# Kernel optimization log

Measured on AMD Instinct MI355X. Metric: run time of the kernel, lower is better.

Reference implementation:

```python
import jax, jax.numpy as jnp
import numpy as np

HIDDEN = 1024
STATE = 16
EXPAND = 2
INNER = HIDDEN * EXPAND
BATCH, SEQ = 4, 2048


def setup_inputs() -> dict:
    key = jax.random.key(0)
    ks = jax.random.split(key, 12)
    s = 0.02
    return {
        "x": jax.random.normal(ks[0], (BATCH, SEQ, HIDDEN), jnp.float32),
        "norm_scale": jnp.ones((HIDDEN,), jnp.float32),
        "norm_bias": jnp.zeros((HIDDEN,), jnp.float32),
        "W_in": jax.random.normal(ks[1], (HIDDEN, 2 * INNER), jnp.float32) * s,
        "conv_w": jax.random.normal(ks[2], (INNER, 3), jnp.float32) * 0.3,
        "conv_b": jnp.zeros((INNER,), jnp.float32),
        "W_dt": jax.random.normal(ks[3], (INNER, INNER), jnp.float32) * s,
        "b_dt": jnp.zeros((INNER,), jnp.float32),
        "A_log": jax.random.normal(ks[4], (INNER, STATE), jnp.float32),
        "D_param": jnp.ones((INNER,), jnp.float32),
        "W_B": jax.random.normal(ks[5], (INNER, STATE), jnp.float32) * s,
        "W_C": jax.random.normal(ks[6], (INNER, STATE), jnp.float32) * s,
        "W_out": jax.random.normal(ks[7], (INNER, HIDDEN), jnp.float32) * s,
    }


def reference(x, norm_scale, norm_bias, W_in, conv_w, conv_b, W_dt, b_dt,
              A_log, D_param, W_B, W_C, W_out):
    residual = x
    # LayerNorm (eps = 1e-5, matches nn.LayerNorm default)
    mu = jnp.mean(x, axis=-1, keepdims=True)
    var = jnp.mean(jnp.square(x - mu), axis=-1, keepdims=True)
    xn = (x - mu) * jax.lax.rsqrt(var + 1e-5) * norm_scale + norm_bias

    xz = xn @ W_in                         # [B, L, 2*inner]
    xb, z = jnp.split(xz, 2, axis=-1)      # each [B, L, inner]

    # depthwise conv1d, kernel 3, padding 1 (cross-correlation as in torch)
    xp = jnp.pad(xb, ((0, 0), (1, 1), (0, 0)))
    xb = (conv_w[:, 0] * xp[:, :-2] + conv_w[:, 1] * xp[:, 1:-1]
          + conv_w[:, 2] * xp[:, 2:] + conv_b)
    xb = jax.nn.silu(xb)

    dt = jax.nn.softplus(xb @ W_dt + b_dt)  # [B, L, inner]
    A = -jnp.exp(A_log)                     # [inner, N]
    Bi = xb @ W_B                           # [B, L, N]
    Ci = xb @ W_C                           # [B, L, N]

    def step(h, inp):
        x_t, dt_t, B_t, C_t = inp           # [B,D], [B,D], [B,N], [B,N]
        A_bar = jnp.exp(dt_t[:, :, None] * A)                 # [B, D, N]
        h = A_bar * h + (dt_t * x_t)[:, :, None] * B_t[:, None, :]
        y_t = jnp.einsum('bdn,bn->bd', h, C_t)
        return h, y_t

    h0 = jnp.zeros((x.shape[0], INNER, STATE), x.dtype)
    xs = (jnp.swapaxes(xb, 0, 1), jnp.swapaxes(dt, 0, 1),
          jnp.swapaxes(Bi, 0, 1), jnp.swapaxes(Ci, 0, 1))
    _, y = jax.lax.scan(step, h0, xs)       # y: [L, B, D]
    y = jnp.swapaxes(y, 0, 1)

    y = (y + D_param * xb) * jax.nn.silu(z)
    return residual + y @ W_out
```

## Files before the change

kernel.cpp:

```cpp
#include <hip/hip_runtime.h>
#include <hip/hip_bf16.h>
#include <cstdint>
#include <cstddef>

#define B_DIM 4
#define L_DIM 2048
#define H_DIM 1024
#define D_DIM 2048
#define N_STATE 16
#define TOKENS (B_DIM * L_DIM)
#define CH 32
#define LC (L_DIM / CH)
#define NEXT 2176

typedef __bf16 bf16x8 __attribute__((ext_vector_type(8)));
typedef float f32x4 __attribute__((ext_vector_type(4)));

__device__ __forceinline__ float sigmoidf_(float x) { return 1.f / (1.f + __expf(-x)); }
__device__ __forceinline__ float softplusf_(float x) {
  return fmaxf(x, 0.f) + log1pf(__expf(-fabsf(x)));
}
__device__ __forceinline__ void gl_lds16(const void* g, void* l) {
  __builtin_amdgcn_global_load_lds(
      (const __attribute__((address_space(1))) unsigned int*)g,
      (__attribute__((address_space(3))) unsigned int*)l, 16, 0, 0);
}

__global__ __launch_bounds__(256) void ln_kernel(const float* __restrict__ x,
    const float* __restrict__ gamma, const float* __restrict__ beta,
    __hip_bfloat16* __restrict__ out) {
  int row = blockIdx.x;
  int t = threadIdx.x;
  const float* px = x + (size_t)row * H_DIM;
  float4 v = *(const float4*)(px + t * 4);
  float s  = v.x + v.y + v.z + v.w;
  float ss = v.x * v.x + v.y * v.y + v.z * v.z + v.w * v.w;
  for (int off = 32; off > 0; off >>= 1) {
    s  += __shfl_down(s, off);
    ss += __shfl_down(ss, off);
  }
  __shared__ float red[8];
  __shared__ float stats[2];
  int wave = t >> 6, lane = t & 63;
  if (lane == 0) { red[wave] = s; red[4 + wave] = ss; }
  __syncthreads();
  if (t == 0) {
    float S  = red[0] + red[1] + red[2] + red[3];
    float SS = red[4] + red[5] + red[6] + red[7];
    float mu = S / H_DIM;
    float var = SS / H_DIM - mu * mu;
    stats[0] = mu;
    stats[1] = rsqrtf(var + 1e-5f);
  }
  __syncthreads();
  float mu = stats[0], rstd = stats[1];
  float4 g  = *(const float4*)(gamma + t * 4);
  float4 bt = *(const float4*)(beta + t * 4);
  __hip_bfloat16* po = out + (size_t)row * H_DIM + t * 4;
  po[0] = __float2bfloat16((v.x - mu) * rstd * g.x + bt.x);
  po[1] = __float2bfloat16((v.y - mu) * rstd * g.y + bt.y);
  po[2] = __float2bfloat16((v.z - mu) * rstd * g.z + bt.z);
  po[3] = __float2bfloat16((v.w - mu) * rstd * g.w + bt.w);
}

__global__ void transpose_bf16(const float* __restrict__ in,
                               __hip_bfloat16* __restrict__ out, int R, int C) {
  __shared__ float tile[32][33];
  int c0 = blockIdx.x * 32, r0 = blockIdx.y * 32;
  int tx = threadIdx.x, ty = threadIdx.y;
  for (int i = 0; i < 32; i += 8)
    tile[ty + i][tx] = in[(size_t)(r0 + ty + i) * C + c0 + tx];
  __syncthreads();
  for (int i = 0; i < 32; i += 8)
    out[(size_t)(c0 + ty + i) * R + r0 + tx] = __float2bfloat16(tile[tx][ty + i]);
}

__global__ __launch_bounds__(256) void wbc_transpose(const float* __restrict__ WB,
    const float* __restrict__ WC, __hip_bfloat16* __restrict__ Wext) {
  int tid = blockIdx.x * 256 + threadIdx.x;
  int c = tid & 31;
  int k0 = (tid >> 5) * 16;
  const float* W = (c < 16) ? WB : WC;
  int cc = c & 15;
  __hip_bfloat16* o = Wext + (size_t)(2048 + c) * D_DIM + k0;
  for (int kk = 0; kk < 16; ++kk)
    o[kk] = __float2bfloat16(W[(size_t)(k0 + kk) * N_STATE + cc]);
}

#define BM 128
#define BN 128
#define BK 64

template <int MODE>
__global__ __launch_bounds__(256) void gemm_bf16(
    const __hip_bfloat16* __restrict__ A, const __hip_bfloat16* __restrict__ Bt,
    void* __restrict__ C0, void* __restrict__ C1, int nsplit,
    int K, int lda, int ldb, int ldc, int gx,
    const float* __restrict__ bias, const float* __restrict__ resid) {
  __shared__ __hip_bfloat16 As[2 * BM * BK];
  __shared__ __hip_bfloat16 Bs[2 * BN * BK];
  int t = threadIdx.x;
  int bid = blockIdx.x;
  int nsup = gx << 3;
  int super = bid / nsup;
  int rem = bid - super * nsup;
  int m0 = (super * 8 + (rem & 7)) * BM;
  int n0 = (rem >> 3) * BN;

  int wave = t >> 6, lane = t & 63;
  int quad = lane >> 4, l16 = lane & 15;
  int wm = (wave >> 1) * 64, wn = (wave & 1) * 64;

  f32x4 acc[4][4] = {};

  int srow  = t >> 3;
  int cslot = t & 7;
  int cdata = cslot ^ (srow & 7);
  const __hip_bfloat16* Ag[4];
  const __hip_bfloat16* Bg[4];
  int soff[4];
#pragma unroll
  for (int j = 0; j < 4; ++j) {
    Ag[j]  = A  + (size_t)(m0 + j * 32 + srow) * lda + cdata * 8;
    Bg[j]  = Bt + (size_t)(n0 + j * 32 + srow) * ldb + cdata * 8;
    soff[j] = (j * 32 + srow) * BK + cslot * 8;
  }

  const int NT = K / BK;
#pragma unroll
  for (int j = 0; j < 4; ++j) {
    gl_lds16(Ag[j], &As[soff[j]]);
    gl_lds16(Bg[j], &Bs[soff[j]]);
  }
  asm volatile("s_waitcnt vmcnt(0)" ::: "memory");
  __builtin_amdgcn_s_barrier();

  for (int kt = 0; kt < NT; ++kt) {
    const int cur = (kt & 1) * (BM * BK);
    const int nxt = cur ^ (BM * BK);
    if (kt + 1 < NT) {
      const int k1 = (kt + 1) * BK;
#pragma unroll
      for (int j = 0; j < 4; ++j) {
        gl_lds16(Ag[j] + k1, &As[nxt + soff[j]]);
        gl_lds16(Bg[j] + k1, &Bs[nxt + soff[j]]);
      }
    }
#pragma unroll
    for (int s = 0; s < 2; ++s) {
      int cs = ((s * 4 + quad) ^ (l16 & 7)) * 8;
      bf16x8 af[4], bf_[4];
#pragma unroll
      for (int i = 0; i < 4; ++i) {
        af[i]  = *(const bf16x8*)&As[cur + (wm + i * 16 + l16) * BK + cs];
        bf_[i] = *(const bf16x8*)&Bs[cur + (wn + i * 16 + l16) * BK + cs];
      }
#pragma unroll
      for (int i = 0; i < 4; ++i)
#pragma unroll
        for (int j = 0; j < 4; ++j)
          acc[i][j] = __builtin_amdgcn_mfma_f32_16x16x32_bf16(af[i], bf_[j], acc[i][j], 0, 0, 0);
    }
    asm volatile("s_waitcnt vmcnt(0)" ::: "memory");
    __builtin_amdgcn_s_barrier();
  }

#pragma unroll
  for (int i = 0; i < 4; ++i) {
    int row0 = m0 + wm + i * 16 + quad * 4;
#pragma unroll
    for (int j = 0; j < 4; ++j) {
      int col = n0 + wn + j * 16 + l16;
      f32x4 v = acc[i][j];
      if (MODE == 0) {
#pragma unroll
        for (int r = 0; r < 4; ++r) {
          size_t idx = (size_t)(row0 + r) * ldc + col;
          ((float*)C0)[idx] = v[r] + resid[idx];
        }
      } else if (MODE == 1) {
        bool mainc = (col < nsplit);
        __hip_bfloat16* cb = mainc ? (__hip_bfloat16*)C0 : (__hip_bfloat16*)C1;
        int ccol = mainc ? col : col - nsplit;
#pragma unroll
        for (int r = 0; r < 4; ++r)
          cb[(size_t)(row0 + r) * ldc + ccol] = __float2bfloat16(v[r]);
      } else {
        if (col < nsplit) {
          float bb = bias[col];
#pragma unroll
          for (int r = 0; r < 4; ++r)
            ((__hip_bfloat16*)C0)[(size_t)(row0 + r) * ldc + col] =
                __float2bfloat16(softplusf_(v[r] + bb));
        } else {
#pragma unroll
          for (int r = 0; r < 4; ++r)
            ((float*)C1)[(size_t)(row0 + r) * 128 + (col - nsplit)] = v[r];
        }
      }
    }
  }
}

__global__ __launch_bounds__(256) void conv_silu_kernel(const __hip_bfloat16* __restrict__ xb,
    const float* __restrict__ cw, const float* __restrict__ cb,
    __hip_bfloat16* __restrict__ xbc) {
  size_t i2 = (size_t)blockIdx.x * 256 + threadIdx.x;
  int dp = (int)(i2 & (D_DIM / 2 - 1));
  size_t tok = i2 >> 10;
  int l = (int)(tok & (L_DIM - 1));
  int d = dp * 2;
  const __hip_bfloat162* base = (const __hip_bfloat162*)xb + i2;
  __hip_bfloat162 cc = base[0];
  float v0 = cw[d * 3 + 1] * __bfloat162float(cc.x) + cb[d];
  float v1 = cw[d * 3 + 4] * __bfloat162float(cc.y) + cb[d + 1];
  if (l > 0) {
    __hip_bfloat162 pm = base[-(D_DIM / 2)];
    v0 += cw[d * 3 + 0] * __bfloat162float(pm.x);
    v1 += cw[d * 3 + 3] * __bfloat162float(pm.y);
  }
  if (l < L_DIM - 1) {
    __hip_bfloat162 pp = base[D_DIM / 2];
    v0 += cw[d * 3 + 2] * __bfloat162float(pp.x);
    v1 += cw[d * 3 + 5] * __bfloat162float(pp.y);
  }
  v0 = v0 * sigmoidf_(v0);
  v1 = v1 * sigmoidf_(v1);
  __hip_bfloat162 o;
  o.x = __float2bfloat16(v0);
  o.y = __float2bfloat16(v1);
  ((__hip_bfloat162*)xbc)[i2] = o;
}

__global__ __launch_bounds__(256) void scan1_kernel(const __hip_bfloat16* __restrict__ dt,
    const __hip_bfloat16* __restrict__ xbc, const float* __restrict__ BiCi,
    const float* __restrict__ A_log, float* __restrict__ hfin,
    float* __restrict__ dtsum) {
  __shared__ float Bsh[LC * N_STATE];
  int t = threadIdx.x;
  int d = blockIdx.x * 256 + t;
  int c = blockIdx.y, b = blockIdx.z;
  size_t base = (size_t)b * L_DIM + (size_t)c * LC;
  for (int idx = t; idx < LC * 4; idx += 256) {
    int row = idx >> 2, q = idx & 3;
    ((float4*)Bsh)[row * 4 + q] = *(const float4*)&BiCi[(base + row) * 128 + q * 4];
  }
  float Aneg[N_STATE];
  {
    const float4* Ap = (const float4*)(A_log + (size_t)d * N_STATE);
#pragma unroll
    for (int q = 0; q < 4; ++q) {
      float4 av = Ap[q];
      Aneg[4 * q + 0] = -__expf(av.x);
      Aneg[4 * q + 1] = -__expf(av.y);
      Aneg[4 * q + 2] = -__expf(av.z);
      Aneg[4 * q + 3] = -__expf(av.w);
    }
  }
  __syncthreads();
  const __hip_bfloat16* dtp = dt + base * D_DIM + d;
  const __hip_bfloat16* xp = xbc + base * D_DIM + d;
  float h[N_STATE];
#pragma unroll
  for (int n = 0; n < N_STATE; ++n) h[n] = 0.f;
  float ds = 0.f;
  float dtv = __bfloat162float(dtp[0]), xv = __bfloat162float(xp[0]);
  for (int i = 0; i < LC; ++i) {
    int ip = (i < LC - 1) ? i + 1 : i;
    float dt2 = __bfloat162float(dtp[(size_t)ip * D_DIM]);
    float x2  = __bfloat162float(xp[(size_t)ip * D_DIM]);
    float dtx = dtv * xv;
    ds += dtv;
    const float4* Brow = (const float4*)&Bsh[i * N_STATE];
#pragma unroll
    for (int q = 0; q < 4; ++q) {
      float4 bv = Brow[q];
      h[4*q+0] = __expf(dtv * Aneg[4*q+0]) * h[4*q+0] + dtx * bv.x;
      h[4*q+1] = __expf(dtv * Aneg[4*q+1]) * h[4*q+1] + dtx * bv.y;
      h[4*q+2] = __expf(dtv * Aneg[4*q+2]) * h[4*q+2] + dtx * bv.z;
      h[4*q+3] = __expf(dtv * Aneg[4*q+3]) * h[4*q+3] + dtx * bv.w;
    }
    dtv = dt2; xv = x2;
  }
  float* ho = hfin + (((size_t)b * CH + c) * D_DIM + d) * N_STATE;
#pragma unroll
  for (int q = 0; q < 4; ++q) {
    float4 v; v.x = h[4*q]; v.y = h[4*q+1]; v.z = h[4*q+2]; v.w = h[4*q+3];
    ((float4*)ho)[q] = v;
  }
  dtsum[((size_t)b * CH + c) * D_DIM + d] = ds;
}

__global__ __launch_bounds__(256) void scan2_kernel(const float* __restrict__ hfin,
    const float* __restrict__ dtsum, const float* __restrict__ A_log,
    float* __restrict__ hstart) {
  int tid = blockIdx.x * 256 + threadIdx.x;
  int n = tid & 15;
  int d = (tid >> 4) & (D_DIM - 1);
  int b = tid >> 15;
  float Aneg = -__expf(A_log[d * N_STATE + n]);
  float run = 0.f;
  for (int c = 0; c < CH; ++c) {
    size_t o = (((size_t)b * CH + c) * D_DIM + d) * N_STATE + n;
    hstart[o] = run;
    run = __expf(Aneg * dtsum[((size_t)b * CH + c) * D_DIM + d]) * run + hfin[o];
  }
}

__global__ __launch_bounds__(256) void scan3_kernel(const __hip_bfloat16* __restrict__ dt,
    const __hip_bfloat16* __restrict__ xbc, const float* __restrict__ BiCi,
    const float* __restrict__ A_log,
    const float* __restrict__ hstart, const __hip_bfloat16* __restrict__ z,
    const float* __restrict__ Dp, __hip_bfloat16* __restrict__ yo) {
  __shared__ float Bsh[LC * N_STATE];
  __shared__ float Csh[LC * N_STATE];
  int t = threadIdx.x;
  int d = blockIdx.x * 256 + t;
  int c = blockIdx.y, b = blockIdx.z;
  size_t base = (size_t)b * L_DIM + (size_t)c * LC;
  for (int idx = t; idx < LC * 4; idx += 256) {
    int row = idx >> 2, q = idx & 3;
    ((float4*)Bsh)[row * 4 + q] = *(const float4*)&BiCi[(base + row) * 128 + q * 4];
    ((float4*)Csh)[row * 4 + q] = *(const float4*)&BiCi[(base + row) * 128 + 16 + q * 4];
  }
  float Aneg[N_STATE];
  {
    const float4* Ap = (const float4*)(A_log + (size_t)d * N_STATE);
#pragma unroll
    for (int q = 0; q < 4; ++q) {
      float4 av = Ap[q];
      Aneg[4 * q + 0] = -__expf(av.x);
      Aneg[4 * q + 1] = -__expf(av.y);
      Aneg[4 * q + 2] = -__expf(av.z);
      Aneg[4 * q + 3] = -__expf(av.w);
    }
  }
  float h[N_STATE];
  {
    const float4* hs = (const float4*)(hstart + (((size_t)b * CH + c) * D_DIM + d) * N_STATE);
#pragma unroll
    for (int q = 0; q < 4; ++q) {
      float4 v = hs[q];
      h[4*q] = v.x; h[4*q+1] = v.y; h[4*q+2] = v.z; h[4*q+3] = v.w;
    }
  }
  float Dv = Dp[d];
  __syncthreads();
  const __hip_bfloat16* dtp = dt + base * D_DIM + d;
  const __hip_bfloat16* xp = xbc + base * D_DIM + d;
  const __hip_bfloat16* zp = z + base * D_DIM + d;
  __hip_bfloat16* yp = yo + base * D_DIM + d;
  float dtv = __bfloat162float(dtp[0]), xv = __bfloat162float(xp[0]);
  float zv = __bfloat162float(zp[0]);
  for (int i = 0; i < LC; ++i) {
    int ip = (i < LC - 1) ? i + 1 : i;
    float dt2 = __bfloat162float(dtp[(size_t)ip * D_DIM]);
    float x2  = __bfloat162float(xp[(size_t)ip * D_DIM]);
    float z2  = __bfloat162float(zp[(size_t)ip * D_DIM]);
    float dtx = dtv * xv;
    const float4* Brow = (const float4*)&Bsh[i * N_STATE];
    const float4* Crow = (const float4*)&Csh[i * N_STATE];
    float yv = 0.f;
#pragma unroll
    for (int q = 0; q < 4; ++q) {
      float4 bv = Brow[q];
      float4 cv = Crow[q];
      h[4*q+0] = __expf(dtv * Aneg[4*q+0]) * h[4*q+0] + dtx * bv.x;
      h[4*q+1] = __expf(dtv * Aneg[4*q+1]) * h[4*q+1] + dtx * bv.y;
      h[4*q+2] = __expf(dtv * Aneg[4*q+2]) * h[4*q+2] + dtx * bv.z;
      h[4*q+3] = __expf(dtv * Aneg[4*q+3]) * h[4*q+3] + dtx * bv.w;
      yv += h[4*q+0] * cv.x + h[4*q+1] * cv.y + h[4*q+2] * cv.z + h[4*q+3] * cv.w;
    }
    float g = zv * sigmoidf_(zv);
    yp[(size_t)i * D_DIM] = __float2bfloat16((yv + Dv * xv) * g);
    dtv = dt2; xv = x2; zv = z2;
  }
}

extern "C" void kernel_launch(void* const* d_in, const int* in_sizes, int n_in,
                              void* d_out, int out_size, void* d_ws, size_t ws_size,
                              hipStream_t stream) {
  const float* x          = (const float*)d_in[0];
  const float* norm_scale = (const float*)d_in[1];
  const float* norm_bias  = (const float*)d_in[2];
  const float* W_in       = (const float*)d_in[3];
  const float* conv_w     = (const float*)d_in[4];
  const float* conv_b     = (const float*)d_in[5];
  const float* W_dt       = (const float*)d_in[6];
  const float* b_dt       = (const float*)d_in[7];
  const float* A_log      = (const float*)d_in[8];
  const float* D_param    = (const float*)d_in[9];
  const float* W_B        = (const float*)d_in[10];
  const float* W_C        = (const float*)d_in[11];
  const float* W_out      = (const float*)d_in[12];
  float* out = (float*)d_out;

  const size_t MB = 1024 * 1024;
  const size_t NEEDED = 193 * MB;
  if (ws_size < NEEDED) return;

  char* ws = (char*)d_ws;
  __hip_bfloat16* xn     = (__hip_bfloat16*)(ws);
  __hip_bfloat16* W_outT = (__hip_bfloat16*)(ws);
  __hip_bfloat16* xb     = (__hip_bfloat16*)(ws + 16 * MB);
  __hip_bfloat16* ybf    = (__hip_bfloat16*)(ws + 16 * MB);
  __hip_bfloat16* z      = (__hip_bfloat16*)(ws + 48 * MB);
  __hip_bfloat16* xbc    = (__hip_bfloat16*)(ws + 80 * MB);
  __hip_bfloat16* dtY    = (__hip_bfloat16*)(ws + 112 * MB);
  float*          BiCi   = (float*)(ws + 144 * MB);
  __hip_bfloat16* W_ext  = (__hip_bfloat16*)(ws + 148 * MB);
  float*          hstart = (float*)(ws + 158 * MB);
  float*          dtsum  = (float*)(ws + 174 * MB);
  __hip_bfloat16* W_inT  = (__hip_bfloat16*)(ws + 177 * MB);
  float*          hfin   = (float*)(ws + 177 * MB);

  dim3 tb(32, 8);
  transpose_bf16<<<dim3(4096 / 32, 1024 / 32), tb, 0, stream>>>(W_in, W_inT, 1024, 4096);
  transpose_bf16<<<dim3(2048 / 32, 2048 / 32), tb, 0, stream>>>(W_dt, W_ext, 2048, 2048);
  wbc_transpose<<<16, 256, 0, stream>>>(W_B, W_C, W_ext);
  ln_kernel<<<TOKENS, 256, 0, stream>>>(x, norm_scale, norm_bias, xn);
  gemm_bf16<1><<<(4096 / BN) * (TOKENS / BM), 256, 0, stream>>>(
      xn, W_inT, xb, z, D_DIM, H_DIM, H_DIM, H_DIM, D_DIM, 4096 / BN,
      nullptr, nullptr);
  transpose_bf16<<<dim3(1024 / 32, 2048 / 32), tb, 0, stream>>>(W_out, W_outT, 2048, 1024);
  conv_silu_kernel<<<(TOKENS * D_DIM / 2) / 256, 256, 0, stream>>>(xb, conv_w, conv_b, xbc);
  gemm_bf16<2><<<(NEXT / BN) * (TOKENS / BM), 256, 0, stream>>>(
      xbc, W_ext, dtY, BiCi, D_DIM, D_DIM, D_DIM, D_DIM, D_DIM, NEXT / BN,
      b_dt, nullptr);
  scan1_kernel<<<dim3(D_DIM / 256, CH, B_DIM), 256, 0, stream>>>(
      dtY, xbc, BiCi, A_log, hfin, dtsum);
  scan2_kernel<<<(B_DIM * D_DIM * N_STATE) / 256, 256, 0, stream>>>(
      hfin, dtsum, A_log, hstart);
  scan3_kernel<<<dim3(D_DIM / 256, CH, B_DIM), 256, 0, stream>>>(
      dtY, xbc, BiCi, A_log, hstart, z, D_param, ybf);
  gemm_bf16<0><<<(H_DIM / BN) * (TOKENS / BM), 256, 0, stream>>>(
      ybf, W_outT, out, nullptr, 1 << 30, D_DIM, D_DIM, D_DIM, H_DIM, H_DIM / BN,
      nullptr, x);
}
```

Measured before the change: 575.5 us.

## Add 256x256-tile bf16 MFMA GEMM and use it for input and dt/B/C projections

Introduces a 512-thread GEMM kernel with 256x256 output tiles, swizzled LDS staging via direct global-to-LDS loads, and double buffering, replacing the 128x128 GEMM for the input projection and the fused dt/B/C projection. Larger tiles raise arithmetic intensity and reduce global traffic per FLOP. The extended-weight width is padded to a multiple of 256, with output writes clipped by a column limit. Risks include lower occupancy from the large LDS footprint and tail imbalance from fewer, larger workgroups.

```diff
diff --git a/kernel.cpp b/kernel.cpp
--- a/kernel.cpp
+++ b/kernel.cpp
@@ -11,7 +11,8 @@
 #define TOKENS (B_DIM * L_DIM)
 #define CH 32
 #define LC (L_DIM / CH)
-#define NEXT 2176
+#define NEXT 2304
+#define NLIM2 2080
 
 typedef __bf16 bf16x8 __attribute__((ext_vector_type(8)));
 typedef float f32x4 __attribute__((ext_vector_type(4)));
@@ -85,6 +86,126 @@
   __hip_bfloat16* o = Wext + (size_t)(2048 + c) * D_DIM + k0;
   for (int kk = 0; kk < 16; ++kk)
     o[kk] = __float2bfloat16(W[(size_t)(k0 + kk) * N_STATE + cc]);
+}
+
+#define BK256 64
+
+template <int MODE>
+__global__ __launch_bounds__(512, 2) void gemm256(
+    const __hip_bfloat16* __restrict__ A, const __hip_bfloat16* __restrict__ Bt,
+    void* __restrict__ C0, void* __restrict__ C1, int nsplit, int nlimit,
+    int K, int lda, int ldb, int ldc, int ntn,
+    const float* __restrict__ bias, const float* __restrict__ resid) {
+  __shared__ __hip_bfloat16 lds[65536];
+  const int t = threadIdx.x;
+  const int nwg = gridDim.x;
+  int bid = blockIdx.x;
+  int wgid = (bid & 7) * (nwg >> 3) + (bid >> 3);
+  const int m0 = (wgid / ntn) * 256;
+  const int n0 = (wgid % ntn) * 256;
+
+  const int wave = t >> 6, lane = t & 63;
+  const int wm = wave >> 2, wn = wave & 3;
+  const int l16 = lane & 15, quad = lane >> 4;
+
+  const int srow = t >> 3, cslot = t & 7;
+  const int cdata = cslot ^ (srow & 7);
+  const __hip_bfloat16* Ag = A + (size_t)(m0 + srow) * lda + cdata * 8;
+  const __hip_bfloat16* Bg = Bt + (size_t)(n0 + srow) * ldb + cdata * 8;
+  const int stoff = srow * 64 + cslot * 8;
+
+  const int aoffs0 = (wm * 128 + l16) * 64 + ((quad ^ (l16 & 7)) * 8);
+  const int aoffs1 = (wm * 128 + l16) * 64 + (((quad + 4) ^ (l16 & 7)) * 8);
+  const int boffs0 = 16384 + (wn * 64 + l16) * 64 + ((quad ^ (l16 & 7)) * 8);
+  const int boffs1 = 16384 + (wn * 64 + l16) * 64 + (((quad + 4) ^ (l16 & 7)) * 8);
+
+  const int NT = K / BK256;
+  f32x4 acc[8][4] = {};
+
+#pragma unroll
+  for (int g = 0; g < 4; ++g) {
+    gl_lds16(Ag + (size_t)g * 64 * lda, &lds[g * 4096 + stoff]);
+    gl_lds16(Bg + (size_t)g * 64 * ldb, &lds[16384 + g * 4096 + stoff]);
+  }
+  asm volatile("s_waitcnt vmcnt(0)" ::: "memory");
+  __builtin_amdgcn_s_barrier();
+
+  for (int kt = 0; kt < NT; ++kt) {
+    const int cur = (kt & 1) << 15;
+    const int nxt = cur ^ 32768;
+    if (kt + 1 < NT) {
+      const int k1 = (kt + 1) * BK256;
+#pragma unroll
+      for (int g = 0; g < 4; ++g) {
+        gl_lds16(Ag + (size_t)g * 64 * lda + k1, &lds[nxt + g * 4096 + stoff]);
+        gl_lds16(Bg + (size_t)g * 64 * ldb + k1, &lds[nxt + 16384 + g * 4096 + stoff]);
+      }
+    }
+    bf16x8 bf_[2][4];
+#pragma unroll
+    for (int j = 0; j < 4; ++j) {
+      bf_[0][j] = *(const bf16x8*)&lds[cur + boffs0 + j * 1024];
+      bf_[1][j] = *(const bf16x8*)&lds[cur + boffs1 + j * 1024];
+    }
+#pragma unroll
+    for (int ip = 0; ip < 4; ++ip) {
+      bf16x8 af[2][2];
+#pragma unroll
+      for (int r = 0; r < 2; ++r) {
+        af[r][0] = *(const bf16x8*)&lds[cur + aoffs0 + (ip * 2 + r) * 1024];
+        af[r][1] = *(const bf16x8*)&lds[cur + aoffs1 + (ip * 2 + r) * 1024];
+      }
+#pragma unroll
+      for (int r = 0; r < 2; ++r)
+#pragma unroll
+        for (int j = 0; j < 4; ++j) {
+          acc[ip * 2 + r][j] = __builtin_amdgcn_mfma_f32_16x16x32_bf16(
+              af[r][0], bf_[0][j], acc[ip * 2 + r][j], 0, 0, 0);
+          acc[ip * 2 + r][j] = __builtin_amdgcn_mfma_f32_16x16x32_bf16(
+              af[r][1], bf_[1][j], acc[ip * 2 + r][j], 0, 0, 0);
+        }
+    }
+    asm volatile("s_waitcnt vmcnt(0)" ::: "memory");
+    __builtin_amdgcn_s_barrier();
+  }
+
+  const int row_base = m0 + wm * 128;
+  const int col_base = n0 + wn * 64;
+#pragma unroll
+  for (int i = 0; i < 8; ++i) {
+    const int row0 = row_base + i * 16 + quad * 4;
+#pragma unroll
+    for (int j = 0; j < 4; ++j) {
+      const int col = col_base + j * 16 + l16;
+      f32x4 v = acc[i][j];
+      if (MODE == 0) {
+#pragma unroll
+        for (int r = 0; r < 4; ++r) {
+          size_t idx = (size_t)(row0 + r) * ldc + col;
+          ((float*)C0)[idx] = v[r] + resid[idx];
+        }
+      } else if (MODE == 1) {
+        bool mainc = (col < nsplit);
+        __hip_bfloat16* cb = mainc ? (__hip_bfloat16*)C0 : (__hip_bfloat16*)C1;
+        int ccol = mainc ? col : col - nsplit;
+#pragma unroll
+        for (int r = 0; r < 4; ++r)
+          cb[(size_t)(row0 + r) * ldc + ccol] = __float2bfloat16(v[r]);
+      } else {
+        if (col < nsplit) {
+          float bb = bias[col];
+#pragma unroll
+          for (int r = 0; r < 4; ++r)
+            ((__hip_bfloat16*)C0)[(size_t)(row0 + r) * ldc + col] =
+                __float2bfloat16(softplusf_(v[r] + bb));
+        } else if (col < nlimit) {
+#pragma unroll
+          for (int r = 0; r < 4; ++r)
+            ((float*)C1)[(size_t)(row0 + r) * 128 + (col - nsplit)] = v[r];
+        }
+      }
+    }
+  }
 }
 
 #define BM 128
@@ -419,13 +540,13 @@
   transpose_bf16<<<dim3(2048 / 32, 2048 / 32), tb, 0, stream>>>(W_dt, W_ext, 2048, 2048);
   wbc_transpose<<<16, 256, 0, stream>>>(W_B, W_C, W_ext);
   ln_kernel<<<TOKENS, 256, 0, stream>>>(x, norm_scale, norm_bias, xn);
-  gemm_bf16<1><<<(4096 / BN) * (TOKENS / BM), 256, 0, stream>>>(
-      xn, W_inT, xb, z, D_DIM, H_DIM, H_DIM, H_DIM, D_DIM, 4096 / BN,
+  gemm256<1><<<(TOKENS / 256) * (4096 / 256), 512, 0, stream>>>(
+      xn, W_inT, xb, z, D_DIM, 1 << 30, H_DIM, H_DIM, H_DIM, D_DIM, 4096 / 256,
       nullptr, nullptr);
   transpose_bf16<<<dim3(1024 / 32, 2048 / 32), tb, 0, stream>>>(W_out, W_outT, 2048, 1024);
   conv_silu_kernel<<<(TOKENS * D_DIM / 2) / 256, 256, 0, stream>>>(xb, conv_w, conv_b, xbc);
-  gemm_bf16<2><<<(NEXT / BN) * (TOKENS / BM), 256, 0, stream>>>(
-      xbc, W_ext, dtY, BiCi, D_DIM, D_DIM, D_DIM, D_DIM, D_DIM, NEXT / BN,
+  gemm256<2><<<(TOKENS / 256) * (NEXT / 256), 512, 0, stream>>>(
+      xbc, W_ext, dtY, BiCi, D_DIM, NLIM2, D_DIM, D_DIM, D_DIM, D_DIM, NEXT / 256,
       b_dt, nullptr);
   scan1_kernel<<<dim3(D_DIM / 256, CH, B_DIM), 256, 0, stream>>>(
       dtY, xbc, BiCi, A_log, hfin, dtsum);
```

After: 656.9 us. 14.1% more time.
